# Optimization experiments

Measured on AMD Instinct MI355X. Metric: run time of the kernel, lower is better.

The kernel has to match this reference:

```python
import jax, jax.numpy as jnp
import numpy as np

N, E, D, H = 100000, 1000000, 128, 8
DH = D // H
SCALE = 1.0 / np.sqrt(DH)


def setup_inputs() -> dict:
    key = jax.random.key(0)
    ks = jax.random.split(key, 12)
    inp = {
        "x": jax.random.normal(ks[0], (N, D), jnp.float32),
        "edge_index": jax.random.randint(ks[1], (2, E), 0, N, dtype=jnp.int64),
        "a": jnp.array(0.25, jnp.float32),  # shared PReLU slope
    }
    names = ["Wq1", "Wk1", "Wv1", "Ws1", "Wq2", "Wk2", "Wv2", "Ws2"]
    for i, n in enumerate(names):
        # kaiming_normal_: std = sqrt(2 / fan_in)
        inp[n] = jax.random.normal(ks[2 + i], (D, D), jnp.float32) * np.sqrt(2.0 / D)
        inp["b" + n[1:]] = jnp.zeros((D,), jnp.float32)
    return inp


def prelu(x, a):
    return jnp.where(x >= 0, x, a * x)


def transformer_conv(x, src, dst, Wq, bq, Wk, bk, Wv, bv, Ws, bs):
    # PyG TransformerConv: query from target (dst), key/value from source (src),
    # scatter-softmax over incoming edges of each dst node, root skip via lin_skip.
    q = (x @ Wq + bq).reshape(N, H, DH)
    k = (x @ Wk + bk).reshape(N, H, DH)
    v = (x @ Wv + bv).reshape(N, H, DH)
    score = jnp.einsum("ehd,ehd->eh", q[dst], k[src]) * SCALE  # [E, H]
    m = jax.lax.stop_gradient(jax.ops.segment_max(score, dst, num_segments=N))  # [N, H]
    e = jnp.exp(score - m[dst])
    s = jax.ops.segment_sum(e, dst, num_segments=N)  # [N, H]
    alpha = e / s[dst]  # scatter-softmax, [E, H]
    agg = jax.ops.segment_sum(alpha[..., None] * v[src], dst, num_segments=N)  # [N, H, DH]
    return agg.reshape(N, D) + x @ Ws + bs


def reference(x, edge_index, a,
              Wq1, bq1, Wk1, bk1, Wv1, bv1, Ws1, bs1,
              Wq2, bq2, Wk2, bk2, Wv2, bv2, Ws2, bs2):
    src, dst = edge_index[0], edge_index[1]
    h = transformer_conv(x, src, dst, Wq1, bq1, Wk1, bk1, Wv1, bv1, Ws1, bs1)
    h = prelu(h, a)
    h = transformer_conv(h, src, dst, Wq2, bq2, Wk2, bk2, Wv2, bv2, Ws2, bs2)
    h = h + x
    return prelu(h, a)
```

## Files before the change

kernel.cpp:

```cpp
#include <hip/hip_runtime.h>
#include <hip/hip_bf16.h>
#include <math.h>

#define D 128
#define SCALE 0.25f
#define NEG_BIG (-1e30f)
#define SLOTS 32

#define BN 256
#define NBMAX 512
#define CAP 7936
#define P1B 256

typedef __attribute__((ext_vector_type(8))) short bf16x8;
typedef __attribute__((ext_vector_type(4))) float f32x4;
typedef __attribute__((ext_vector_type(2))) float f32x2;

__device__ inline __hip_bfloat162 pack2(float a, float b) {
    __hip_bfloat162 h;
    h.x = __float2bfloat16(a);
    h.y = __float2bfloat16(b);
    return h;
}

__device__ __forceinline__ float dot4_bf16(float qx, float qy, float kx, float ky) {
    __hip_bfloat162 q01 = *(__hip_bfloat162*)&qx, q23 = *(__hip_bfloat162*)&qy;
    __hip_bfloat162 k01 = *(__hip_bfloat162*)&kx, k23 = *(__hip_bfloat162*)&ky;
    return __bfloat162float(q01.x) * __bfloat162float(k01.x)
         + __bfloat162float(q01.y) * __bfloat162float(k01.y)
         + __bfloat162float(q23.x) * __bfloat162float(k23.x)
         + __bfloat162float(q23.y) * __bfloat162float(k23.y);
}

__device__ inline int detect_is64(const int* __restrict__ ei) {
    int lane = threadIdx.x & 63;
    int v = ei[2 * lane + 1];
    unsigned long long b = __ballot(v != 0);
    return b == 0ULL;
}

struct PackArgs { const float* w[8]; };

__global__ __launch_bounds__(256) void prep_phase1(
    PackArgs pa, __hip_bfloat16* __restrict__ WtP,
    const float* __restrict__ x, __hip_bfloat16* __restrict__ xb, int n4,
    const int* __restrict__ ei, int E, int NB,
    int* __restrict__ gcount, unsigned long long* __restrict__ bucketbuf)
{
    __shared__ int hist[NBMAX];
    __shared__ int lbase[NBMAX];
    __shared__ int lcur[NBMAX];

    int b = blockIdx.x;
    int tid = threadIdx.x;
    if (b < 8) {
        const float* W = pa.w[b];
        __hip_bfloat16* dst = WtP + (size_t)b * 128 * 128;
        for (int idx = tid; idx < 128 * 128; idx += 256) {
            int c = idx & 127, k = idx >> 7;
            dst[(size_t)c * 128 + k] = __float2bfloat16(W[(size_t)k * 128 + c]);
        }
        return;
    }
    if (b < 8 + P1B) {
        int blk = b - 8;
        int is64 = detect_is64(ei);
        int slice = (E + P1B - 1) / P1B;
        int base = blk * slice;
        int lim = base + slice; if (lim > E) lim = E;

        for (int i = tid; i < NB; i += 256) { hist[i] = 0; lcur[i] = 0; }
        __syncthreads();

        for (int e = base + tid; e < lim; e += 256) {
            int d = is64 ? ei[2 * E + 2 * e] : ei[E + e];
            atomicAdd(&hist[d >> 8], 1);
        }
        __syncthreads();

        for (int i = tid; i < NB; i += 256) {
            int h = hist[i];
            lbase[i] = h ? atomicAdd(&gcount[i], h) : 0;
        }
        __syncthreads();

        for (int e = base + tid; e < lim; e += 256) {
            int s = is64 ? ei[2 * e]         : ei[e];
            int d = is64 ? ei[2 * E + 2 * e] : ei[E + e];
            int bb = d >> 8;
            int pos = lbase[bb] + atomicAdd(&lcur[bb], 1);
            if (pos < CAP)
                bucketbuf[(size_t)bb * CAP + pos] =
                    ((unsigned long long)(unsigned)d << 32) | (unsigned)s;
        }
        return;
    }
    {
        int i = (b - 8 - P1B) * 256 + tid;
        if (i < n4) {
            float4 v = ((const float4*)x)[i];
            __hip_bfloat162 h0 = pack2(v.x, v.y), h1 = pack2(v.z, v.w);
            f32x2 st; st[0] = *(float*)&h0; st[1] = *(float*)&h1;
            __builtin_nontemporal_store(st, (f32x2*)((__hip_bfloat162*)xb + 2 * i));
        }
    }
}

#define TSTR 136

__device__ __forceinline__ void gemm_body(
    int bx, __hip_bfloat16* bufA, __hip_bfloat16* bufB,
    const __hip_bfloat16* __restrict__ A, const __hip_bfloat16* __restrict__ Wt,
    const float* __restrict__ bq, const float* __restrict__ bk,
    const float* __restrict__ bv, const float* __restrict__ bs,
    __hip_bfloat16* __restrict__ qb, __hip_bfloat16* __restrict__ kv,
    __hip_bfloat16* __restrict__ skipb, int M)
{
    const int tid = threadIdx.x;
    const int w = tid >> 6, lane = tid & 63;
    const int wr = w >> 1, wc = w & 1;
    const int blk0 = bx * 64;
    const int rowBase = blk0 + wr * 32;
    const int l16 = lane & 15;
    const int quad = lane >> 4;

    bf16x8 xfrag[2][4];
    #pragma unroll
    for (int i = 0; i < 2; ++i) {
        int r = rowBase + i * 16 + l16;
        if (r >= M) r = M - 1;
        #pragma unroll
        for (int kb = 0; kb < 4; ++kb)
            xfrag[i][kb] = __builtin_nontemporal_load(
                (const bf16x8*)(A + (size_t)r * D + kb * 32 + quad * 8));
    }

    const float* biases[4] = {bq, bk, bv, bs};

    for (int cb = 0; cb < 4; ++cb) {
        const __hip_bfloat16* Wblk = Wt + (size_t)cb * 128 * 128;
        f32x4 acc[2][4];
        #pragma unroll
        for (int i = 0; i < 2; i++)
            #pragma unroll
            for (int jt = 0; jt < 4; jt++) acc[i][jt] = (f32x4){0.f, 0.f, 0.f, 0.f};

        #pragma unroll
        for (int kb = 0; kb < 4; ++kb) {
            const int k0 = kb * 32 + quad * 8;
            #pragma unroll
            for (int jt = 0; jt < 4; ++jt) {
                int c = wc * 64 + jt * 16 + l16;
                bf16x8 wfrag = *(const bf16x8*)(Wblk + (size_t)c * D + k0);
                acc[0][jt] = __builtin_amdgcn_mfma_f32_16x16x32_bf16(wfrag, xfrag[0][kb], acc[0][jt], 0, 0, 0);
                acc[1][jt] = __builtin_amdgcn_mfma_f32_16x16x32_bf16(wfrag, xfrag[1][kb], acc[1][jt], 0, 0, 0);
            }
        }

        __hip_bfloat16* dst = (cb == 2) ? bufB : bufA;
        const float* bias = biases[cb];
        #pragma unroll
        for (int jt = 0; jt < 4; ++jt) {
            int c0 = wc * 64 + jt * 16 + quad * 4;
            float4 bb = *(const float4*)(bias + c0);
            #pragma unroll
            for (int i = 0; i < 2; ++i) {
                int lrow = wr * 32 + i * 16 + l16;
                f32x4 vv = acc[i][jt];
                __hip_bfloat162 h0 = pack2(vv[0] + bb.x, vv[1] + bb.y);
                __hip_bfloat162 h1 = pack2(vv[2] + bb.z, vv[3] + bb.w);
                float2 st; st.x = *(float*)&h0; st.y = *(float*)&h1;
                *(float2*)(&dst[lrow * TSTR + c0]) = st;
            }
        }

        if (cb == 1) continue;

        __syncthreads();

        if (cb == 0 || cb == 3) {
            __hip_bfloat16* gout = (cb == 0) ? qb : skipb;
            #pragma unroll
            for (int it = 0; it < 4; ++it) {
                int lrow = it * 16 + (tid >> 4);
                int grow = blk0 + lrow;
                if (grow < M) {
                    f32x4 vv = *(const f32x4*)(&bufA[lrow * TSTR + (tid & 15) * 8]);
                    __builtin_nontemporal_store(vv,
                        (f32x4*)(gout + (size_t)grow * D + (tid & 15) * 8));
                }
            }
        } else {
            #pragma unroll
            for (int it = 0; it < 8; ++it) {
                int lrow = it * 8 + (tid >> 5);
                int grow = blk0 + lrow;
                int g = tid & 31;
                if (grow < M) {
                    float2 kk = *(const float2*)(&bufA[lrow * TSTR + g * 4]);
                    float2 vv = *(const float2*)(&bufB[lrow * TSTR + g * 4]);
                    float4 o; o.x = kk.x; o.y = kk.y; o.z = vv.x; o.w = vv.y;
                    *(float4*)(kv + (size_t)grow * 256 + g * 8) = o;
                }
            }
        }
        __syncthreads();
    }
}

__global__ __launch_bounds__(256) void gemm_mfma(
    const __hip_bfloat16* __restrict__ A, const __hip_bfloat16* __restrict__ Wt,
    const float* __restrict__ bq, const float* __restrict__ bk,
    const float* __restrict__ bv, const float* __restrict__ bs,
    __hip_bfloat16* __restrict__ qb, __hip_bfloat16* __restrict__ kv,
    __hip_bfloat16* __restrict__ skipb, int M)
{
    __shared__ __hip_bfloat16 smem[2 * 64 * TSTR];
    gemm_body(blockIdx.x, smem, smem + 64 * TSTR, A, Wt, bq, bk, bv, bs, qb, kv, skipb, M);
}

__global__ __launch_bounds__(256) void csr_gemm1(
    const __hip_bfloat16* __restrict__ A, const __hip_bfloat16* __restrict__ Wt,
    const float* __restrict__ bq, const float* __restrict__ bk,
    const float* __restrict__ bv, const float* __restrict__ bs,
    __hip_bfloat16* __restrict__ qb, __hip_bfloat16* __restrict__ kv,
    __hip_bfloat16* __restrict__ skipb, int M,
    const int* __restrict__ gcount, const unsigned long long* __restrict__ bucketbuf,
    int NB,
    int* __restrict__ deg, int* __restrict__ slots,
    unsigned long long* __restrict__ ovf, int* __restrict__ ovfcnt)
{
    __shared__ __hip_bfloat16 smem[2 * 64 * TSTR];
    const int bx = blockIdx.x;
    const int tid = threadIdx.x;

    if (bx < NB) {
        int* ldeg  = (int*)smem;
        int* lslot = ldeg + BN;

        int cnt = gcount[bx]; if (cnt > CAP) cnt = CAP;
        ldeg[tid] = 0;
        __syncthreads();

        const unsigned long long* bb = bucketbuf + (size_t)bx * CAP;
        for (int i = tid; i < cnt; i += 256) {
            unsigned long long e = bb[i];
            int d = (int)(e >> 32);
            int s = (int)(e & 0xffffffffULL);
            int ln = d & (BN - 1);
            int pos = atomicAdd(&ldeg[ln], 1);
            if (pos < SLOTS) {
                lslot[ln * SLOTS + pos] = s;
            } else {
                int op = atomicAdd(ovfcnt, 1);
                ovf[op] = e;
            }
        }
        __syncthreads();

        int n0 = bx << 8;
        if (n0 + tid < M) deg[n0 + tid] = ldeg[tid];
        for (int i = tid; i < BN * SLOTS / 4; i += 256) {
            int node = n0 + (i >> 3);
            if (node < M)
                ((int4*)slots)[(size_t)n0 * 8 + i] = ((int4*)lslot)[i];
        }
        __syncthreads();
    }

    gemm_body(bx, smem, smem + 64 * TSTR, A, Wt, bq, bk, bv, bs, qb, kv, skipb, M);
}

__device__ inline void store4(float* base, size_t off, float o0, float o1, float o2, float o3) {
    f32x4 v; v[0] = o0; v[1] = o1; v[2] = o2; v[3] = o3;
    __builtin_nontemporal_store(v, (f32x4*)(base + off));
}
__device__ inline void store4(__hip_bfloat16* base, size_t off, float o0, float o1, float o2, float o3) {
    __hip_bfloat162 h0 = pack2(o0, o1), h1 = pack2(o2, o3);
    f32x2 st; st[0] = *(float*)&h0; st[1] = *(float*)&h1;
    __builtin_nontemporal_store(st, (f32x2*)(base + off));
}

template <typename OutT>
__global__ __launch_bounds__(256) void attn_agg(
    const __hip_bfloat16* __restrict__ qb, const __hip_bfloat16* __restrict__ kv,
    const int* __restrict__ deg, const int* __restrict__ slots,
    const unsigned long long* __restrict__ ovf, const int* __restrict__ ovfcnt,
    const __hip_bfloat16* __restrict__ skip, const __hip_bfloat16* __restrict__ residb,
    const float* __restrict__ a_ptr, OutT* __restrict__ out, int Nn) {
    int tid = threadIdx.x;
    int lane = tid & 63;
    int half = lane >> 5;
    int lh = lane & 31;
    int n = blockIdx.x * 8 + (tid >> 6) * 2 + half;
    bool valid = (n < Nn);
    int nc = valid ? n : (Nn - 1);
    const float a = a_ptr[0];

    int myslot = __builtin_nontemporal_load(slots + nc * SLOTS + lh);
    myslot = ((unsigned)myslot < (unsigned)Nn) ? myslot : 0;

    f32x2 qraw = __builtin_nontemporal_load((const f32x2*)(qb + (size_t)nc * D + 4 * lh));
    float qx = qraw[0], qy = qraw[1];

    float s = 0.f, A0 = 0.f, A1 = 0.f, A2 = 0.f, A3 = 0.f;

    int cnt = valid ? __builtin_nontemporal_load(deg + nc) : 0;
    int cmain = min(cnt, SLOTS);
    int cmax = max(cmain, __shfl_xor(cmain, 32));

    const float4* kvp4 = (const float4*)kv;

    for (int t = 0; t < cmax; t += 8) {
        float4 f[8];
        float sc[8];
        #pragma unroll
        for (int i = 0; i < 8; ++i) {
            int sval = __shfl(myslot, half * 32 + t + i);
            int src = (t + i < cmain) ? sval : 0;
            f[i] = kvp4[(size_t)src * 32 + lh];
        }
        #pragma unroll
        for (int i = 0; i < 8; ++i) {
            float p = dot4_bf16(qx, qy, f[i].x, f[i].y);
            p += __shfl_xor(p, 1);
            p += __shfl_xor(p, 2);
            sc[i] = (t + i < cmain) ? p * SCALE : NEG_BIG;
        }
        #pragma unroll
        for (int i = 0; i < 8; ++i) {
            float wgt = __expf(sc[i]);
            __hip_bfloat162 v01 = *(__hip_bfloat162*)&f[i].z;
            __hip_bfloat162 v23 = *(__hip_bfloat162*)&f[i].w;
            A0 += wgt * __bfloat162float(v01.x);
            A1 += wgt * __bfloat162float(v01.y);
            A2 += wgt * __bfloat162float(v23.x);
            A3 += wgt * __bfloat162float(v23.y);
            s += wgt;
        }
    }

    if (__any(cnt > SLOTS)) {
        int oc = *ovfcnt;
        for (int i = 0; i < oc; ++i) {
            unsigned long long e = ovf[i];
            int dd = (int)(e >> 32);
            int ss = (int)(e & 0xffffffffULL);
            bool take = (dd == nc) && (cnt > SLOTS) && valid;
            ss = ((unsigned)ss < (unsigned)Nn) ? ss : 0;
            float4 fo = kvp4[(size_t)ss * 32 + lh];
            float p = dot4_bf16(qx, qy, fo.x, fo.y);
            p += __shfl_xor(p, 1);
            p += __shfl_xor(p, 2);
            float wgt = take ? __expf(p * SCALE) : 0.f;
            __hip_bfloat162 v01 = *(__hip_bfloat162*)&fo.z;
            __hip_bfloat162 v23 = *(__hip_bfloat162*)&fo.w;
            A0 += wgt * __bfloat162float(v01.x);
            A1 += wgt * __bfloat162float(v01.y);
            A2 += wgt * __bfloat162float(v23.x);
            A3 += wgt * __bfloat162float(v23.y);
            s += wgt;
        }
    }

    if (!valid) return;
    float inv = (cnt > 0) ? 1.f / s : 0.f;
    f32x2 skr = __builtin_nontemporal_load((const f32x2*)(skip + (size_t)n * D + 4 * lh));
    float skx = skr[0], sky = skr[1];
    __hip_bfloat162 s01 = *(__hip_bfloat162*)&skx;
    __hip_bfloat162 s23 = *(__hip_bfloat162*)&sky;
    float o0 = A0 * inv + __bfloat162float(s01.x);
    float o1 = A1 * inv + __bfloat162float(s01.y);
    float o2 = A2 * inv + __bfloat162float(s23.x);
    float o3 = A3 * inv + __bfloat162float(s23.y);
    if (residb) {
        f32x2 rr = __builtin_nontemporal_load((const f32x2*)(residb + (size_t)n * D + 4 * lh));
        float rx = rr[0], ry = rr[1];
        __hip_bfloat162 r01 = *(__hip_bfloat162*)&rx;
        __hip_bfloat162 r23 = *(__hip_bfloat162*)&ry;
        o0 += __bfloat162float(r01.x);
        o1 += __bfloat162float(r01.y);
        o2 += __bfloat162float(r23.x);
        o3 += __bfloat162float(r23.y);
    }
    o0 = (o0 >= 0.f) ? o0 : a * o0;
    o1 = (o1 >= 0.f) ? o1 : a * o1;
    o2 = (o2 >= 0.f) ? o2 : a * o2;
    o3 = (o3 >= 0.f) ? o3 : a * o3;
    store4(out, (size_t)n * D + 4 * lh, o0, o1, o2, o3);
}

extern "C" void kernel_launch(void* const* d_in, const int* in_sizes, int n_in,
                              void* d_out, int out_size, void* d_ws, size_t ws_size,
                              hipStream_t stream) {
    const float* x  = (const float*)d_in[0];
    const int*   ei = (const int*)d_in[1];
    const float* a  = (const float*)d_in[2];
    const float* Wq1 = (const float*)d_in[3];  const float* bq1 = (const float*)d_in[4];
    const float* Wk1 = (const float*)d_in[5];  const float* bk1 = (const float*)d_in[6];
    const float* Wv1 = (const float*)d_in[7];  const float* bv1 = (const float*)d_in[8];
    const float* Ws1 = (const float*)d_in[9];  const float* bs1 = (const float*)d_in[10];
    const float* Wq2 = (const float*)d_in[11]; const float* bq2 = (const float*)d_in[12];
    const float* Wk2 = (const float*)d_in[13]; const float* bk2 = (const float*)d_in[14];
    const float* Wv2 = (const float*)d_in[15]; const float* bv2 = (const float*)d_in[16];
    const float* Ws2 = (const float*)d_in[17]; const float* bs2 = (const float*)d_in[18];

    const int N = in_sizes[0] / D;
    const int E = in_sizes[1] / 2;
    const size_t NF = (size_t)N * D;
    const int NB = (N + BN - 1) / BN;

    char* wp = (char*)d_ws;
    __hip_bfloat16* xb    = (__hip_bfloat16*)wp; wp += NF * 2;
    __hip_bfloat16* h1b   = (__hip_bfloat16*)wp; wp += NF * 2;
    __hip_bfloat16* qb    = (__hip_bfloat16*)wp; wp += NF * 2;
    __hip_bfloat16* kv    = (__hip_bfloat16*)wp; wp += NF * 4;
    __hip_bfloat16* skipb = (__hip_bfloat16*)wp; wp += NF * 2;
    __hip_bfloat16* WtP   = (__hip_bfloat16*)wp; wp += 2 * 512 * 128 * 2;
    int* deg    = (int*)wp;                wp += (size_t)N * 4;
    int* ovfcnt = (int*)wp;                wp += 64;
    int* gcount = (int*)wp;                wp += NBMAX * 4;
    size_t zbytes = 64 + NBMAX * 4;
    int* slots  = (int*)wp;                wp += (size_t)N * SLOTS * 4;
    unsigned long long* ovf = (unsigned long long*)wp; wp += (size_t)E * 8;
    unsigned long long* bucketbuf = (unsigned long long*)h1b;
    float* out = (float*)d_out;

    const int TB = 256;
    int gGemm = (N + 63) / 64;
    int gAttn = (N + 7) / 8;
    int n4 = (int)(NF / 4);
    int gCvt = (n4 + TB - 1) / TB;

    PackArgs pa;
    pa.w[0] = Wq1; pa.w[1] = Wk1; pa.w[2] = Wv1; pa.w[3] = Ws1;
    pa.w[4] = Wq2; pa.w[5] = Wk2; pa.w[6] = Wv2; pa.w[7] = Ws2;

    (void)hipMemsetAsync(ovfcnt, 0, zbytes, stream);

    hipLaunchKernelGGL(prep_phase1, dim3(8 + P1B + gCvt), dim3(TB), 0, stream,
                       pa, WtP, x, xb, n4, ei, E, NB, gcount, bucketbuf);

    hipLaunchKernelGGL(csr_gemm1, dim3(gGemm), dim3(TB), 0, stream,
                       xb, WtP, bq1, bk1, bv1, bs1, qb, kv, skipb, N,
                       gcount, bucketbuf, NB, deg, slots, ovf, ovfcnt);
    hipLaunchKernelGGL(attn_agg<__hip_bfloat16>, dim3(gAttn), dim3(TB), 0, stream,
                       qb, kv, deg, slots, ovf, ovfcnt, skipb,
                       (const __hip_bfloat16*)nullptr, a, h1b, N);

    hipLaunchKernelGGL(gemm_mfma, dim3(gGemm), dim3(TB), 0, stream,
                       h1b, WtP + 512 * 128, bq2, bk2, bv2, bs2, qb, kv, skipb, N);
    hipLaunchKernelGGL(attn_agg<float>, dim3(gAttn), dim3(TB), 0, stream,
                       qb, kv, deg, slots, ovf, ovfcnt, skipb, xb, a, out, N);
}
```

Baseline: 467.4 us.

## Halve GEMM LDS staging, shrink CSR buckets to 128 nodes, tile weight transpose

The GEMM epilogue now uses a single 64-row LDS staging buffer instead of two, writing the K and V halves into the interleaved kv array in separate passes. The aim is to halve shared memory per block and raise occupancy. CSR bucketing moves from 256 to 128 nodes per bucket, which doubles the bucket count so the CSR work spreads over more blocks, and adjusts the capacity. The weight transpose goes through a padded 32x33 LDS tile so both global reads and writes coalesce. In exchange the kv stores become narrower, strided 8-byte writes, and there is an extra sync per column block.

```diff
diff --git a/kernel.cpp b/kernel.cpp
--- a/kernel.cpp
+++ b/kernel.cpp
@@ -7,9 +7,9 @@
 #define NEG_BIG (-1e30f)
 #define SLOTS 32
 
-#define BN 256
-#define NBMAX 512
-#define CAP 7936
+#define BN 128
+#define NBMAX 1024
+#define CAP 4080
 #define P1B 256
 
 typedef __attribute__((ext_vector_type(8))) short bf16x8;
@@ -50,15 +50,26 @@
     __shared__ int hist[NBMAX];
     __shared__ int lbase[NBMAX];
     __shared__ int lcur[NBMAX];
+    __shared__ float wt[32][33];
 
     int b = blockIdx.x;
     int tid = threadIdx.x;
     if (b < 8) {
         const float* W = pa.w[b];
         __hip_bfloat16* dst = WtP + (size_t)b * 128 * 128;
-        for (int idx = tid; idx < 128 * 128; idx += 256) {
-            int c = idx & 127, k = idx >> 7;
-            dst[(size_t)c * 128 + k] = __float2bfloat16(W[(size_t)k * 128 + c]);
+        int row = tid >> 5, col = tid & 31;
+        for (int t = 0; t < 16; ++t) {
+            int tr = (t >> 2) * 32, tc = (t & 3) * 32;
+            #pragma unroll
+            for (int p = 0; p < 4; ++p)
+                wt[p * 8 + row][col] = W[(size_t)(tr + p * 8 + row) * 128 + tc + col];
+            __syncthreads();
+            #pragma unroll
+            for (int p = 0; p < 4; ++p) {
+                int i = p * 8 + row;
+                dst[(size_t)(tc + i) * 128 + tr + col] = __float2bfloat16(wt[col][i]);
+            }
+            __syncthreads();
         }
         return;
     }
@@ -74,7 +85,7 @@
 
         for (int e = base + tid; e < lim; e += 256) {
             int d = is64 ? ei[2 * E + 2 * e] : ei[E + e];
-            atomicAdd(&hist[d >> 8], 1);
+            atomicAdd(&hist[d >> 7], 1);
         }
         __syncthreads();
 
@@ -87,7 +98,7 @@
         for (int e = base + tid; e < lim; e += 256) {
             int s = is64 ? ei[2 * e]         : ei[e];
             int d = is64 ? ei[2 * E + 2 * e] : ei[E + e];
-            int bb = d >> 8;
+            int bb = d >> 7;
             int pos = lbase[bb] + atomicAdd(&lcur[bb], 1);
             if (pos < CAP)
                 bucketbuf[(size_t)bb * CAP + pos] =
@@ -109,7 +120,7 @@
 #define TSTR 136
 
 __device__ __forceinline__ void gemm_body(
-    int bx, __hip_bfloat16* bufA, __hip_bfloat16* bufB,
+    int bx, __hip_bfloat16* buf,
     const __hip_bfloat16* __restrict__ A, const __hip_bfloat16* __restrict__ Wt,
     const float* __restrict__ bq, const float* __restrict__ bk,
     const float* __restrict__ bv, const float* __restrict__ bs,
@@ -157,7 +168,6 @@
             }
         }
 
-        __hip_bfloat16* dst = (cb == 2) ? bufB : bufA;
         const float* bias = biases[cb];
         #pragma unroll
         for (int jt = 0; jt < 4; ++jt) {
@@ -170,11 +180,9 @@
                 __hip_bfloat162 h0 = pack2(vv[0] + bb.x, vv[1] + bb.y);
                 __hip_bfloat162 h1 = pack2(vv[2] + bb.z, vv[3] + bb.w);
                 float2 st; st.x = *(float*)&h0; st.y = *(float*)&h1;
-                *(float2*)(&dst[lrow * TSTR + c0]) = st;
-            }
-        }
-
-        if (cb == 1) continue;
+                *(float2*)(&buf[lrow * TSTR + c0]) = st;
+            }
+        }
 
         __syncthreads();
 
@@ -185,22 +193,21 @@
                 int lrow = it * 16 + (tid >> 4);
                 int grow = blk0 + lrow;
                 if (grow < M) {
-                    f32x4 vv = *(const f32x4*)(&bufA[lrow * TSTR + (tid & 15) * 8]);
+                    f32x4 vv = *(const f32x4*)(&buf[lrow * TSTR + (tid & 15) * 8]);
                     __builtin_nontemporal_store(vv,
                         (f32x4*)(gout + (size_t)grow * D + (tid & 15) * 8));
                 }
             }
         } else {
+            int voff = (cb == 2) ? 4 : 0;
             #pragma unroll
             for (int it = 0; it < 8; ++it) {
                 int lrow = it * 8 + (tid >> 5);
                 int grow = blk0 + lrow;
                 int g = tid & 31;
                 if (grow < M) {
-                    float2 kk = *(const float2*)(&bufA[lrow * TSTR + g * 4]);
-                    float2 vv = *(const float2*)(&bufB[lrow * TSTR + g * 4]);
-                    float4 o; o.x = kk.x; o.y = kk.y; o.z = vv.x; o.w = vv.y;
-                    *(float4*)(kv + (size_t)grow * 256 + g * 8) = o;
+                    float2 hv = *(const float2*)(&buf[lrow * TSTR + g * 4]);
+                    *(float2*)(kv + (size_t)grow * 256 + g * 8 + voff) = hv;
                 }
             }
         }
@@ -215,8 +222,8 @@
     __hip_bfloat16* __restrict__ qb, __hip_bfloat16* __restrict__ kv,
     __hip_bfloat16* __restrict__ skipb, int M)
 {
-    __shared__ __hip_bfloat16 smem[2 * 64 * TSTR];
-    gemm_body(blockIdx.x, smem, smem + 64 * TSTR, A, Wt, bq, bk, bv, bs, qb, kv, skipb, M);
+    __shared__ __hip_bfloat16 smem[64 * TSTR];
+    gemm_body(blockIdx.x, smem, A, Wt, bq, bk, bv, bs, qb, kv, skipb, M);
 }
 
 __global__ __launch_bounds__(256) void csr_gemm1(
@@ -230,7 +237,7 @@
     int* __restrict__ deg, int* __restrict__ slots,
     unsigned long long* __restrict__ ovf, int* __restrict__ ovfcnt)
 {
-    __shared__ __hip_bfloat16 smem[2 * 64 * TSTR];
+    __shared__ __hip_bfloat16 smem[64 * TSTR];
     const int bx = blockIdx.x;
     const int tid = threadIdx.x;
 
@@ -239,7 +246,7 @@
         int* lslot = ldeg + BN;
 
         int cnt = gcount[bx]; if (cnt > CAP) cnt = CAP;
-        ldeg[tid] = 0;
+        if (tid < BN) ldeg[tid] = 0;
         __syncthreads();
 
         const unsigned long long* bb = bucketbuf + (size_t)bx * CAP;
@@ -258,8 +265,8 @@
         }
         __syncthreads();
 
-        int n0 = bx << 8;
-        if (n0 + tid < M) deg[n0 + tid] = ldeg[tid];
+        int n0 = bx << 7;
+        if (tid < BN && n0 + tid < M) deg[n0 + tid] = ldeg[tid];
         for (int i = tid; i < BN * SLOTS / 4; i += 256) {
             int node = n0 + (i >> 3);
             if (node < M)
@@ -268,7 +275,7 @@
         __syncthreads();
     }
 
-    gemm_body(bx, smem, smem + 64 * TSTR, A, Wt, bq, bk, bv, bs, qb, kv, skipb, M);
+    gemm_body(bx, smem, A, Wt, bq, bk, bv, bs, qb, kv, skipb, M);
 }
 
 __device__ inline void store4(float* base, size_t off, float o0, float o1, float o2, float o3) {
```

Result: slower. 495.0 us (+5.9%).
